# Kernel optimization log

Hardware: AMD Instinct MI355X
Metric: run time of the kernel (lower is better)

The kernel has to match this reference:

```python
import jax, jax.numpy as jnp
import numpy as np

N_ENT = 100000   # entities per KG
N_EDGE = 500000  # edges per KG
N_SEED = 10000
DIM = 128


def _norm_adj(edges, n):
    # edges: [E,2] int. Build undirected adjacency + self loops, sym deg^-1/2 norm.
    loop = jnp.arange(n)
    src = jnp.concatenate([edges[:, 0], edges[:, 1], loop])
    dst = jnp.concatenate([edges[:, 1], edges[:, 0], loop])
    deg = jax.ops.segment_sum(jnp.ones(src.shape[0], jnp.float32), dst, num_segments=n)
    norm = jax.lax.rsqrt(deg[src] * deg[dst])  # [E_tot]
    return src, dst, norm


def _gcn(x, edges, Ws, n):
    # MultiLayerGCN: per layer H = relu(A_norm @ X @ W + X) (residual=True)
    src, dst, norm = _norm_adj(edges, n)
    for W in Ws:
        agg = jax.ops.segment_sum(x[src] * norm[:, None], dst, num_segments=n)  # [n,d]
        x = jax.nn.relu(agg @ W + x)
    return x


def setup_inputs() -> dict:
    key = jax.random.key(0)
    ks = jax.random.split(key, 10)
    return {
        "sr_ent_seeds": jax.random.randint(ks[0], (N_SEED,), 0, N_ENT),
        "tg_ent_seeds": jax.random.randint(ks[1], (N_SEED,), 0, N_ENT),
        "triples_sr": jax.random.randint(ks[2], (N_EDGE, 3), 0, N_ENT),
        "triples_tg": jax.random.randint(ks[3], (N_EDGE, 3), 0, N_ENT),
        "embedding_sr": jax.random.normal(ks[4], (N_ENT, DIM), jnp.float32),
        "embedding_tg": jax.random.normal(ks[5], (N_ENT, DIM), jnp.float32),
        "edges_sr": jax.random.randint(ks[6], (N_EDGE, 2), 0, N_ENT),
        "edges_tg": jax.random.randint(ks[7], (N_EDGE, 2), 0, N_ENT),
        "W1": jax.random.normal(ks[8], (DIM, DIM), jnp.float32) * (DIM ** -0.5),
        "W2": jax.random.normal(ks[9], (DIM, DIM), jnp.float32) * (DIM ** -0.5),
    }


def reference(sr_ent_seeds, tg_ent_seeds, triples_sr, triples_tg,
              embedding_sr, embedding_tg, edges_sr, edges_tg, W1, W2):
    Ws = [W1, W2]
    sr_ent_hid = _gcn(embedding_sr, edges_sr, Ws, N_ENT)
    tg_ent_hid = _gcn(embedding_tg, edges_tg, Ws, N_ENT)
    sr_seed_hid = sr_ent_hid[sr_ent_seeds]
    tg_seed_hid = tg_ent_hid[tg_ent_seeds]
    return (sr_seed_hid, tg_seed_hid, sr_ent_hid, tg_ent_hid)
```

## Files before the change

### kernel.cpp

```cpp
#include <hip/hip_runtime.h>
#include <hip/hip_bf16.h>

#define N_ENT_C   100000
#define N_EDGE_C  500000
#define N_SEED_C  10000
#define DIM_C     128

#define N2_C      (2 * N_ENT_C)
#define NBKT      391
#define BKT_CAP   8192
#define EPB       2048

typedef unsigned int   u32;
typedef unsigned short u16;
typedef __attribute__((ext_vector_type(8))) short bf16x8;
typedef __attribute__((ext_vector_type(4))) float f32x4;

__device__ __forceinline__ float bflo(u32 v) { return __uint_as_float(v << 16); }
__device__ __forceinline__ float bfhi(u32 v) { return __uint_as_float(v & 0xFFFF0000u); }
__device__ __forceinline__ u16 f2bf(float f) {
  u32 u = __float_as_uint(f);
  u += 0x7FFFu + ((u >> 16) & 1u);
  return (u16)(u >> 16);
}

__global__ void k_detect(const u32* __restrict__ words, int* __restrict__ flag,
                         int* __restrict__ bkt_cnt) {
  int tid = threadIdx.x;
  bkt_cnt[tid] = 0;
  bkt_cnt[tid + 256] = 0;
  if (tid == 0) {
    int cnt = 0;
    for (int i = 0; i < 64; ++i) {
      u32 e = (words[i] >> 7) & 0xFF;
      cnt += (e < 96) ? 1 : 0;
    }
    *flag = (cnt >= 8) ? 1 : 0;
  }
}

__global__ __launch_bounds__(256, 4) void k_fill_binned(
    const int2* __restrict__ ea, const int2* __restrict__ eb,
    int* __restrict__ bkt_cnt, u32* __restrict__ csr_tmp, int E) {
  __shared__ u32 ein[2 * EPB];
  __shared__ u16 ebkt[2 * EPB];
  __shared__ int lcount[512];
  __shared__ int lstart[513];
  __shared__ int gbase[512];
  __shared__ int ssc[256];

  const int tid = threadIdx.x;
  const int gofs = blockIdx.y ? N_ENT_C : 0;
  const int2* ed = blockIdx.y ? eb : ea;
  const int e0 = blockIdx.x * EPB;

  lcount[tid] = 0; lcount[tid + 256] = 0;
  __syncthreads();

  int2 ev[EPB / 256];
#pragma unroll
  for (int i = 0; i < EPB / 256; ++i) {
    int e = e0 + tid + i * 256;
    int2 v = (e < E) ? ed[e] : make_int2(0, 0);
    ev[i] = v;
    if (e < E) {
      atomicAdd(&lcount[(gofs + v.y) >> 9], 1);
      atomicAdd(&lcount[(gofs + v.x) >> 9], 1);
    }
  }
  __syncthreads();

  int a = lcount[2 * tid], b = lcount[2 * tid + 1];
  int ts = a + b;
  ssc[tid] = ts;
  __syncthreads();
  for (int off = 1; off < 256; off <<= 1) {
    int v = (tid >= off) ? ssc[tid - off] : 0;
    __syncthreads();
    ssc[tid] += v;
    __syncthreads();
  }
  int ex = ssc[tid] - ts;
  lstart[2 * tid] = ex;
  lstart[2 * tid + 1] = ex + a;
  if (tid == 255) lstart[512] = ssc[255];
  __syncthreads();

  {
    int b0 = 2 * tid, b1 = 2 * tid + 1;
    if (b0 < NBKT) { int c = lstart[b0 + 1] - lstart[b0]; gbase[b0] = c ? atomicAdd(&bkt_cnt[b0], c) : 0; }
    if (b1 < NBKT) { int c = lstart[b1 + 1] - lstart[b1]; gbase[b1] = c ? atomicAdd(&bkt_cnt[b1], c) : 0; }
    lcount[tid] = lstart[tid];
    lcount[tid + 256] = lstart[tid + 256];
  }
  __syncthreads();

#pragma unroll
  for (int i = 0; i < EPB / 256; ++i) {
    int e = e0 + tid + i * 256;
    if (e >= E) continue;
    int2 v = ev[i];
    int r1 = gofs + v.y;
    u32 w1 = (u32)v.x | ((u32)(r1 & 511) << 20);
    int bk1 = r1 >> 9;
    int p = atomicAdd(&lcount[bk1], 1);
    ein[p] = w1; ebkt[p] = (u16)bk1;
    int r2 = gofs + v.x;
    u32 w2 = (u32)v.y | ((u32)(r2 & 511) << 20);
    int bk2 = r2 >> 9;
    p = atomicAdd(&lcount[bk2], 1);
    ein[p] = w2; ebkt[p] = (u16)bk2;
  }
  __syncthreads();

  int tot = lstart[512];
  for (int j = tid; j < tot; j += 256) {
    int bk = ebkt[j];
    u32 off = (u32)(gbase[bk] + (j - lstart[bk]));
    if (off < BKT_CAP) csr_tmp[(size_t)bk * BKT_CAP + off] = ein[j];
  }
}

__global__ void k_deg(const u32* __restrict__ csr_tmp, const int* __restrict__ bkt_cnt,
                      float* __restrict__ rdeg) {
  __shared__ int lcnt[512];
  int bk = blockIdx.x, tid = threadIdx.x;
  lcnt[tid] = 0;
  __syncthreads();
  int cnt = min(bkt_cnt[bk], BKT_CAP);
  const u32* src = csr_tmp + (size_t)bk * BKT_CAP;
  for (int j = tid; j < cnt; j += 512)
    atomicAdd(&lcnt[(src[j] >> 20) & 511], 1);
  __syncthreads();
  int row = (bk << 9) + tid;
  if (row < N2_C) rdeg[row] = rsqrtf((float)(lcnt[tid] + 1));
}

__global__ void k_scanb(const int* __restrict__ bkt_cnt, int* __restrict__ bbase,
                        int* __restrict__ row_start) {
  __shared__ int s[512];
  int tid = threadIdx.x;
  int v = (tid < NBKT) ? bkt_cnt[tid] : 0;
  s[tid] = v;
  __syncthreads();
  for (int off = 1; off < 512; off <<= 1) {
    int u = (tid >= off) ? s[tid - off] : 0;
    __syncthreads();
    s[tid] += u;
    __syncthreads();
  }
  if (tid < NBKT) bbase[tid] = s[tid] - v;
  if (tid == NBKT - 1) row_start[N2_C] = s[tid];
}

__global__ __launch_bounds__(512) void k_csr_sort(
    const u32* __restrict__ csr_tmp, const int* __restrict__ bkt_cnt,
    const int* __restrict__ bbase, int* __restrict__ row_start,
    u32* __restrict__ csr) {
  __shared__ int lcnt[512];
  __shared__ int lofs[512];
  int bk = blockIdx.x, tid = threadIdx.x;
  lcnt[tid] = 0;
  __syncthreads();
  int cnt = min(bkt_cnt[bk], BKT_CAP);
  int base = bbase[bk];
  const u32* srcp = csr_tmp + (size_t)bk * BKT_CAP;
  for (int j = tid; j < cnt; j += 512)
    atomicAdd(&lcnt[(srcp[j] >> 20) & 511], 1);
  __syncthreads();
  int own = lcnt[tid];
  lofs[tid] = own;
  __syncthreads();
  for (int off = 1; off < 512; off <<= 1) {
    int u = (tid >= off) ? lofs[tid - off] : 0;
    __syncthreads();
    lofs[tid] += u;
    __syncthreads();
  }
  int ex = lofs[tid] - own;
  int row = (bk << 9) + tid;
  if (row < N2_C) row_start[row] = base + ex;
  lcnt[tid] = ex;
  __syncthreads();
  for (int j = tid; j < cnt; j += 512) {
    u32 w = srcp[j];
    int dl = (w >> 20) & 511;
    int pos = atomicAdd(&lcnt[dl], 1);
    csr[base + pos] = w & 0x1FFFF;
  }
}

__global__ void k_cvt_bf16(const void* __restrict__ s0, const void* __restrict__ s1,
                           u32* __restrict__ d0, u32* __restrict__ d1,
                           const int* __restrict__ flag, int n4) {
  int i = blockIdx.x * 256 + threadIdx.x;
  if (i >= n4) return;
  const void* src = blockIdx.y ? s1 : s0;
  u32* dst = blockIdx.y ? d1 : d0;
  uint4 o;
  if (*flag) {
    const float4* sf = (const float4*)src;
    float4 va = sf[2 * i], vb = sf[2 * i + 1];
    o.x = (u32)f2bf(va.x) | ((u32)f2bf(va.y) << 16);
    o.y = (u32)f2bf(va.z) | ((u32)f2bf(va.w) << 16);
    o.z = (u32)f2bf(vb.x) | ((u32)f2bf(vb.y) << 16);
    o.w = (u32)f2bf(vb.z) | ((u32)f2bf(vb.w) << 16);
  } else {
    o = ((const uint4*)src)[i];
  }
  ((uint4*)dst)[i] = o;
}

#define G2(cp, t, a0, a1) { \
  u32 s0 = __builtin_amdgcn_readfirstlane(cp[t]); \
  u32 s1 = __builtin_amdgcn_readfirstlane(cp[(t) + 1]); \
  float r0 = rdb[s0], r1 = rdb[s1]; \
  u32 v0 = xin[(s0 << 6) | lane]; \
  u32 v1 = xin[(s1 << 6) | lane]; \
  a0 += r0 * bflo(v0) + r1 * bflo(v1); \
  a1 += r0 * bfhi(v0) + r1 * bfhi(v1); }
#define G1(cp, t, a0, a1) { \
  u32 s0 = __builtin_amdgcn_readfirstlane(cp[t]); \
  float r0 = rdb[s0]; \
  u32 v0 = xin[(s0 << 6) | lane]; \
  a0 += r0 * bflo(v0); a1 += r0 * bfhi(v0); }

__global__ __launch_bounds__(512, 8) void k_fused(
    const int* __restrict__ row_start, const u32* __restrict__ csru,
    const u32* __restrict__ xin0, const u32* __restrict__ xin1,
    const float* __restrict__ rdeg, const void* __restrict__ W,
    const int* __restrict__ flag, u32* __restrict__ xout0, u32* __restrict__ xout1,
    float* __restrict__ fout0, float* __restrict__ fout1) {
  __shared__ __align__(16) u16 smem[128 * 128 + 32 * 128];
  u16* sWt = smem;
  u16* sA  = smem + 128 * 128;

  const int tid = threadIdx.x;
  const int row0 = blockIdx.x * 32;
  const int gofs = blockIdx.y * N_ENT_C;
  const u32* __restrict__ xin  = blockIdx.y ? xin1  : xin0;
  u32* __restrict__ xout       = blockIdx.y ? xout1 : xout0;
  float* __restrict__ fout     = blockIdx.y ? fout1 : fout0;
  const int* rsb = row_start + gofs;
  const float* rdb = rdeg + gofs;
  const int isf32 = *flag;

  {
    u32* sW32 = (u32*)sWt;
    const float* Wf = (const float*)W;
    const u16*   Wu = (const u16*)W;
    for (int i = tid; i < 64 * 128; i += 512) {
      int k2 = i >> 7;
      int n  = i & 127;
      u16 lo, hi;
      if (isf32) { lo = f2bf(Wf[(2 * k2) * 128 + n]); hi = f2bf(Wf[(2 * k2 + 1) * 128 + n]); }
      else       { lo = Wu[(2 * k2) * 128 + n];       hi = Wu[(2 * k2 + 1) * 128 + n]; }
      sW32[n * 64 + (k2 ^ ((n & 7) << 2))] = (u32)lo | ((u32)hi << 16);
    }
  }

  const int wave = tid >> 6, lane = tid & 63;
  for (int pq = 0; pq < 2; ++pq) {
    const int rlA = wave * 4 + 2 * pq, rlB = rlA + 1;
    const int rowA = row0 + rlA, rowB = row0 + rlB;
    int rsA = __builtin_amdgcn_readfirstlane(rsb[rowA]);
    int rsB = __builtin_amdgcn_readfirstlane(rsb[rowA + 1]);
    int reB = __builtin_amdgcn_readfirstlane(rsb[rowA + 2]);
    const int deA = rsB - rsA, deB = reB - rsB;
    const float rdA = rdb[rowA], rdB = rdb[rowB];
    const u32 vsA = xin[((u32)rowA << 6) | lane];
    const u32 vsB = xin[((u32)rowB << 6) | lane];
    const u32* cA = csru + rsA;
    const u32* cB = csru + rsB;
    float a0A = 0.f, a1A = 0.f, a0B = 0.f, a1B = 0.f;
    int tA = 0, tB = 0;
    while (tA + 1 < deA && tB + 1 < deB) {
      u32 iA0 = __builtin_amdgcn_readfirstlane(cA[tA]);
      u32 iA1 = __builtin_amdgcn_readfirstlane(cA[tA + 1]);
      u32 iB0 = __builtin_amdgcn_readfirstlane(cB[tB]);
      u32 iB1 = __builtin_amdgcn_readfirstlane(cB[tB + 1]);
      float rA0 = rdb[iA0], rA1 = rdb[iA1];
      float rB0 = rdb[iB0], rB1 = rdb[iB1];
      u32 uA0 = xin[(iA0 << 6) | lane];
      u32 uA1 = xin[(iA1 << 6) | lane];
      u32 uB0 = xin[(iB0 << 6) | lane];
      u32 uB1 = xin[(iB1 << 6) | lane];
      a0A += rA0 * bflo(uA0) + rA1 * bflo(uA1);
      a1A += rA0 * bfhi(uA0) + rA1 * bfhi(uA1);
      a0B += rB0 * bflo(uB0) + rB1 * bflo(uB1);
      a1B += rB0 * bfhi(uB0) + rB1 * bfhi(uB1);
      tA += 2; tB += 2;
    }
    for (; tA + 3 < deA; tA += 4) { G2(cA, tA, a0A, a1A); G2(cA, tA + 2, a0A, a1A); }
    if (tA + 1 < deA) { G2(cA, tA, a0A, a1A); tA += 2; }
    if (tA < deA) G1(cA, tA, a0A, a1A);
    for (; tB + 3 < deB; tB += 4) { G2(cB, tB, a0B, a1B); G2(cB, tB + 2, a0B, a1B); }
    if (tB + 1 < deB) { G2(cB, tB, a0B, a1B); tB += 2; }
    if (tB < deB) G1(cB, tB, a0B, a1B);

    a0A = rdA * a0A + rdA * rdA * bflo(vsA);
    a1A = rdA * a1A + rdA * rdA * bfhi(vsA);
    a0B = rdB * a0B + rdB * rdB * bflo(vsB);
    a1B = rdB * a1B + rdB * rdB * bfhi(vsB);
    ((u32*)sA)[rlA * 64 + (lane ^ ((rlA & 7) << 2))] = (u32)f2bf(a0A) | ((u32)f2bf(a1A) << 16);
    ((u32*)sA)[rlB * 64 + (lane ^ ((rlB & 7) << 2))] = (u32)f2bf(a0B) | ((u32)f2bf(a1B) << 16);
  }
  __syncthreads();

  const int rows_h = (wave >> 2) * 16;
  const int col_q  = (wave & 3) * 32;
  const int m = lane & 15, q = lane >> 4;
  f32x4 acc[2];
  for (int ct = 0; ct < 2; ++ct) acc[ct] = (f32x4){0.f, 0.f, 0.f, 0.f};
#pragma unroll
  for (int kt = 0; kt < 4; ++kt) {
    int k0 = kt * 32 + q * 8;
    int ks = k0 ^ ((m & 7) << 3);
    bf16x8 a = *(const bf16x8*)&sA[(rows_h + m) * 128 + ks];
#pragma unroll
    for (int ct = 0; ct < 2; ++ct) {
      bf16x8 b = *(const bf16x8*)&sWt[(col_q + ct * 16 + m) * 128 + ks];
      acc[ct] = __builtin_amdgcn_mfma_f32_16x16x32_bf16(a, b, acc[ct], 0, 0, 0);
    }
  }
  __syncthreads();

  float* sC = (float*)smem;
#pragma unroll
  for (int ct = 0; ct < 2; ++ct)
#pragma unroll
    for (int r = 0; r < 4; ++r)
      sC[(rows_h + q * 4 + r) * 132 + (col_q + ct * 16 + m)] = acc[ct][r];
  __syncthreads();

  {
    int rowl = tid >> 4;
    int c0 = (tid & 15) * 8;
    int row = row0 + rowl;
    size_t goff = (size_t)row * 64 + (c0 >> 1);
    const u32* resp = xin + goff;
    if (fout) {
      float* op = fout + (size_t)row * 128 + c0;
#pragma unroll
      for (int u2 = 0; u2 < 2; ++u2) {
        u32 rv0 = resp[2 * u2], rv1 = resp[2 * u2 + 1];
        f32x4 f;
        f[0] = fmaxf(sC[rowl * 132 + c0 + 4 * u2    ] + bflo(rv0), 0.f);
        f[1] = fmaxf(sC[rowl * 132 + c0 + 4 * u2 + 1] + bfhi(rv0), 0.f);
        f[2] = fmaxf(sC[rowl * 132 + c0 + 4 * u2 + 2] + bflo(rv1), 0.f);
        f[3] = fmaxf(sC[rowl * 132 + c0 + 4 * u2 + 3] + bfhi(rv1), 0.f);
        __builtin_nontemporal_store(f, (f32x4*)(op + 4 * u2));
      }
    } else {
      u32 ov[4];
#pragma unroll
      for (int u = 0; u < 4; ++u) {
        u32 rv = resp[u];
        float lo = fmaxf(sC[rowl * 132 + c0 + 2 * u]     + bflo(rv), 0.f);
        float hi = fmaxf(sC[rowl * 132 + c0 + 2 * u + 1] + bfhi(rv), 0.f);
        ov[u] = (u32)f2bf(lo) | ((u32)f2bf(hi) << 16);
      }
      uint4* op = (uint4*)(xout + goff);
      op[0] = make_uint4(ov[0], ov[1], ov[2], ov[3]);
    }
  }
}

__global__ void k_out_seed(const float4* __restrict__ ea, const float4* __restrict__ eb,
                           const int* __restrict__ sa, const int* __restrict__ sb,
                           float4* __restrict__ oa, float4* __restrict__ ob, int total4) {
  int t = blockIdx.x * 256 + threadIdx.x;
  if (t >= total4) return;
  const float4* e = blockIdx.y ? eb : ea;
  const int* seeds = blockIdx.y ? sb : sa;
  float4* o = blockIdx.y ? ob : oa;
  int s = t >> 5, w = t & 31;
  o[t] = e[((size_t)seeds[s] << 5) | w];
}

extern "C" void kernel_launch(void* const* d_in, const int* in_sizes, int n_in,
                              void* d_out, int out_size, void* d_ws, size_t ws_size,
                              hipStream_t stream) {
  const int*  sr_seeds = (const int*)d_in[0];
  const int*  tg_seeds = (const int*)d_in[1];
  const void* emb_sr   = d_in[4];
  const void* emb_tg   = d_in[5];
  const int*  edges_sr = (const int*)d_in[6];
  const int*  edges_tg = (const int*)d_in[7];
  const void* W1       = d_in[8];
  const void* W2       = d_in[9];
  float* out = (float*)d_out;

  const int nd = N_ENT_C * DIM_C;

  u16* x_A       = (u16*)d_ws;
  u16* x_B       = x_A + (size_t)nd;
  float* ws_rdeg = (float*)(x_B + (size_t)nd);
  int* ws_flag   = (int*)(ws_rdeg + N2_C);
  int* row_start = ws_flag + 64;
  int* bkt_cnt   = row_start + N2_C + 64;
  int* bbase     = bkt_cnt + 512;
  u32* csr       = (u32*)(bbase + 512);
  u32* csr_tmp   = csr + (size_t)4 * N_EDGE_C;
  u16* x_C       = (u16*)csr_tmp;

  float* out_seed_sr = out;
  float* out_seed_tg = out + (size_t)N_SEED_C * DIM_C;
  float* out_ent_sr  = out + (size_t)2 * N_SEED_C * DIM_C;
  float* out_ent_tg  = out_ent_sr + (size_t)nd;

  u16* x_D = (u16*)out_ent_sr;

  k_detect<<<1, 256, 0, stream>>>((const u32*)emb_sr, ws_flag, bkt_cnt);

  dim3 agrid((N_EDGE_C + EPB - 1) / EPB, 2);
  k_fill_binned<<<agrid, 256, 0, stream>>>((const int2*)edges_sr, (const int2*)edges_tg,
                                           bkt_cnt, csr_tmp, N_EDGE_C);
  k_deg  <<<NBKT, 512, 0, stream>>>(csr_tmp, bkt_cnt, ws_rdeg);
  k_scanb<<<1, 512, 0, stream>>>(bkt_cnt, bbase, row_start);
  k_csr_sort<<<NBKT, 512, 0, stream>>>(csr_tmp, bkt_cnt, bbase, row_start, csr);

  dim3 cgrid((nd / 8 + 255) / 256, 2);
  k_cvt_bf16<<<cgrid, 256, 0, stream>>>(emb_sr, emb_tg, (u32*)x_A, (u32*)x_B, ws_flag, nd / 8);

  const int NBF = N_ENT_C / 32;

  dim3 f2grid(NBF, 2);
  k_fused<<<f2grid, 512, 0, stream>>>(row_start, csr, (const u32*)x_A, (const u32*)x_B,
                                      ws_rdeg, W1, ws_flag, (u32*)x_C, (u32*)x_D,
                                      nullptr, nullptr);

  k_fused<<<dim3(NBF, 1), 512, 0, stream>>>(row_start + N_ENT_C, csr,
                                            (const u32*)x_D, nullptr, ws_rdeg + N_ENT_C,
                                            W2, ws_flag, nullptr, nullptr,
                                            out_ent_tg, nullptr);
  k_fused<<<dim3(NBF, 1), 512, 0, stream>>>(row_start, csr,
                                            (const u32*)x_C, nullptr, ws_rdeg,
                                            W2, ws_flag, nullptr, nullptr,
                                            out_ent_sr, nullptr);

  dim3 sgrid((N_SEED_C * 32 + 255) / 256, 2);
  k_out_seed<<<sgrid, 256, 0, stream>>>((const float4*)out_ent_sr, (const float4*)out_ent_tg,
                                        sr_seeds, tg_seeds,
                                        (float4*)out_seed_sr, (float4*)out_seed_tg,
                                        N_SEED_C * 32);
}
```

Baseline: 523.5 us.

## Fuse bf16 conversion into edge binning and degree into CSR sort

The embedding bf16 conversion now runs as extra blocks of the edge-binning kernel, and the inverse-sqrt degree is computed inside the CSR sort from its per-row counts. This removes two kernel launches and the separate pass that reread the binned edges to count degrees. In exchange, the conversion blocks share a launch with the heavier binning blocks, and nd/8/256 is floor division, which is exact only because nd/8 is a multiple of 256.

Result: faster. 506.3 us (-3.3%).

```diff
diff --git a/kernel.cpp b/kernel.cpp
--- a/kernel.cpp
+++ b/kernel.cpp
@@ -10,6 +10,7 @@
 #define NBKT      391
 #define BKT_CAP   8192
 #define EPB       2048
+#define NB_FILL   ((N_EDGE_C + EPB - 1) / EPB)
 
 typedef unsigned int   u32;
 typedef unsigned short u16;
@@ -39,9 +40,12 @@
   }
 }
 
-__global__ __launch_bounds__(256, 4) void k_fill_binned(
+__global__ __launch_bounds__(256, 4) void k_build(
     const int2* __restrict__ ea, const int2* __restrict__ eb,
-    int* __restrict__ bkt_cnt, u32* __restrict__ csr_tmp, int E) {
+    int* __restrict__ bkt_cnt, u32* __restrict__ csr_tmp, int E,
+    const void* __restrict__ s0, const void* __restrict__ s1,
+    u32* __restrict__ d0, u32* __restrict__ d1,
+    const int* __restrict__ flag, int n4) {
   __shared__ u32 ein[2 * EPB];
   __shared__ u16 ebkt[2 * EPB];
   __shared__ int lcount[512];
@@ -50,6 +54,27 @@
   __shared__ int ssc[256];
 
   const int tid = threadIdx.x;
+
+  if (blockIdx.x >= NB_FILL) {
+    int i = (blockIdx.x - NB_FILL) * 256 + tid;
+    if (i >= n4) return;
+    const void* src = blockIdx.y ? s1 : s0;
+    u32* dst = blockIdx.y ? d1 : d0;
+    uint4 o;
+    if (*flag) {
+      const float4* sf = (const float4*)src;
+      float4 va = sf[2 * i], vb = sf[2 * i + 1];
+      o.x = (u32)f2bf(va.x) | ((u32)f2bf(va.y) << 16);
+      o.y = (u32)f2bf(va.z) | ((u32)f2bf(va.w) << 16);
+      o.z = (u32)f2bf(vb.x) | ((u32)f2bf(vb.y) << 16);
+      o.w = (u32)f2bf(vb.z) | ((u32)f2bf(vb.w) << 16);
+    } else {
+      o = ((const uint4*)src)[i];
+    }
+    ((uint4*)dst)[i] = o;
+    return;
+  }
+
   const int gofs = blockIdx.y ? N_ENT_C : 0;
   const int2* ed = blockIdx.y ? eb : ea;
   const int e0 = blockIdx.x * EPB;
@@ -121,21 +146,6 @@
   }
 }
 
-__global__ void k_deg(const u32* __restrict__ csr_tmp, const int* __restrict__ bkt_cnt,
-                      float* __restrict__ rdeg) {
-  __shared__ int lcnt[512];
-  int bk = blockIdx.x, tid = threadIdx.x;
-  lcnt[tid] = 0;
-  __syncthreads();
-  int cnt = min(bkt_cnt[bk], BKT_CAP);
-  const u32* src = csr_tmp + (size_t)bk * BKT_CAP;
-  for (int j = tid; j < cnt; j += 512)
-    atomicAdd(&lcnt[(src[j] >> 20) & 511], 1);
-  __syncthreads();
-  int row = (bk << 9) + tid;
-  if (row < N2_C) rdeg[row] = rsqrtf((float)(lcnt[tid] + 1));
-}
-
 __global__ void k_scanb(const int* __restrict__ bkt_cnt, int* __restrict__ bbase,
                         int* __restrict__ row_start) {
   __shared__ int s[512];
@@ -156,7 +166,7 @@
 __global__ __launch_bounds__(512) void k_csr_sort(
     const u32* __restrict__ csr_tmp, const int* __restrict__ bkt_cnt,
     const int* __restrict__ bbase, int* __restrict__ row_start,
-    u32* __restrict__ csr) {
+    float* __restrict__ rdeg, u32* __restrict__ csr) {
   __shared__ int lcnt[512];
   __shared__ int lofs[512];
   int bk = blockIdx.x, tid = threadIdx.x;
@@ -179,7 +189,10 @@
   }
   int ex = lofs[tid] - own;
   int row = (bk << 9) + tid;
-  if (row < N2_C) row_start[row] = base + ex;
+  if (row < N2_C) {
+    row_start[row] = base + ex;
+    rdeg[row] = rsqrtf((float)(own + 1));
+  }
   lcnt[tid] = ex;
   __syncthreads();
   for (int j = tid; j < cnt; j += 512) {
@@ -188,27 +201,6 @@
     int pos = atomicAdd(&lcnt[dl], 1);
     csr[base + pos] = w & 0x1FFFF;
   }
-}
-
-__global__ void k_cvt_bf16(const void* __restrict__ s0, const void* __restrict__ s1,
-                           u32* __restrict__ d0, u32* __restrict__ d1,
-                           const int* __restrict__ flag, int n4) {
-  int i = blockIdx.x * 256 + threadIdx.x;
-  if (i >= n4) return;
-  const void* src = blockIdx.y ? s1 : s0;
-  u32* dst = blockIdx.y ? d1 : d0;
-  uint4 o;
-  if (*flag) {
-    const float4* sf = (const float4*)src;
-    float4 va = sf[2 * i], vb = sf[2 * i + 1];
-    o.x = (u32)f2bf(va.x) | ((u32)f2bf(va.y) << 16);
-    o.y = (u32)f2bf(va.z) | ((u32)f2bf(va.w) << 16);
-    o.z = (u32)f2bf(vb.x) | ((u32)f2bf(vb.y) << 16);
-    o.w = (u32)f2bf(vb.z) | ((u32)f2bf(vb.w) << 16);
-  } else {
-    o = ((const uint4*)src)[i];
-  }
-  ((uint4*)dst)[i] = o;
 }
 
 #define G2(cp, t, a0, a1) { \
@@ -413,15 +405,13 @@
 
   k_detect<<<1, 256, 0, stream>>>((const u32*)emb_sr, ws_flag, bkt_cnt);
 
-  dim3 agrid((N_EDGE_C + EPB - 1) / EPB, 2);
-  k_fill_binned<<<agrid, 256, 0, stream>>>((const int2*)edges_sr, (const int2*)edges_tg,
-                                           bkt_cnt, csr_tmp, N_EDGE_C);
-  k_deg  <<<NBKT, 512, 0, stream>>>(csr_tmp, bkt_cnt, ws_rdeg);
+  dim3 bgrid(NB_FILL + nd / 8 / 256, 2);
+  k_build<<<bgrid, 256, 0, stream>>>((const int2*)edges_sr, (const int2*)edges_tg,
+                                     bkt_cnt, csr_tmp, N_EDGE_C,
+                                     emb_sr, emb_tg, (u32*)x_A, (u32*)x_B,
+                                     ws_flag, nd / 8);
   k_scanb<<<1, 512, 0, stream>>>(bkt_cnt, bbase, row_start);
-  k_csr_sort<<<NBKT, 512, 0, stream>>>(csr_tmp, bkt_cnt, bbase, row_start, csr);
-
-  dim3 cgrid((nd / 8 + 255) / 256, 2);
-  k_cvt_bf16<<<cgrid, 256, 0, stream>>>(emb_sr, emb_tg, (u32*)x_A, (u32*)x_B, ws_flag, nd / 8);
+  k_csr_sort<<<NBKT, 512, 0, stream>>>(csr_tmp, bkt_cnt, bbase, row_start, ws_rdeg, csr);
 
   const int NBF = N_ENT_C / 32;
 
```
